# Kernel optimization log

Hardware: AMD Instinct MI355X
Metric: run time of the kernel (lower is better)

## Reference

```python
import jax, jax.numpy as jnp
import numpy as np
import math

L = 2          # gnn_num_layers
NDIM = 256     # gnn_hidden_size
H = 8          # num_heads
HH = H // 2    # heads per (full, local) split
DK = NDIM // H # 32, also == edim (relation_share_heads)
EDIM = DK
B, NPB = 32, 128
N = B * NPB            # 4096 nodes
EF = B * NPB * NPB     # 524288 complete-graph edges
EL = 131072            # local-graph edges
ELG = 262144           # line-graph edges
R = 128                # relation vocab


def _ln(x, g, b, eps=1e-5):
    m = x.mean(-1, keepdims=True)
    v = ((x - m) ** 2).mean(-1, keepdims=True)
    return (x - m) / jnp.sqrt(v + eps) * g + b


def _ffn(x, W1, b1, W2, b2, g, b):
    h = jax.nn.relu(x @ W1 + b1)
    return _ln(x + h @ W2 + b2, g, b)


def _edge_attn(q, k, v, e, src, dst, n_seg):
    """Relation-aware graph attention (DGL propagate_attention + edge_softmax).
    q,k,v: [n_seg,h,d]; e: [E,h,d] edge-relation bias or None; src,dst: [E].
    score_e = ((k[src]+e) . q[dst]) / sqrt(d); softmax over in-edges of dst;
    out[dst] = sum alpha_e * (v[src]+e)."""
    ks = k[src] + e if e is not None else k[src]          # [E,h,d]
    vs = v[src] + e if e is not None else v[src]          # [E,h,d]
    s = jnp.einsum('ehd,ehd->eh', ks, q[dst]) / math.sqrt(q.shape[-1])
    smax = jax.ops.segment_max(s, dst, num_segments=n_seg)
    ex = jnp.exp(s - jnp.maximum(smax, -1e30)[dst])
    den = jax.ops.segment_sum(ex, dst, num_segments=n_seg)[dst]
    alpha = ex / jnp.where(den > 0, den, 1.0)
    return jax.ops.segment_sum(alpha[..., None] * vs, dst, num_segments=n_seg)


def _model(x, rel_embed,
           n_Wq, n_bq, n_Wk, n_bk, n_Wv, n_bv, n_Wo, n_bo, n_ln_g, n_ln_b,
           n_f_W1, n_f_b1, n_f_W2, n_f_b2, n_f_ln_g, n_f_ln_b,
           e_Wsrc, e_Wdst, e_Wq, e_bq, e_Wk, e_Wv, e_Wo, e_bo, e_ln_g, e_ln_b,
           e_f_W1, e_f_b1, e_f_W2, e_f_b2, e_f_ln_g, e_f_ln_b,
           full_src, full_dst, g_src, g_dst, lg_src, lg_dst, edge_feat, full_edge_feat):
    lg_x = rel_embed[edge_feat]            # [EL, EDIM]  (shared embedding)
    lg_x_full = rel_embed[full_edge_feat]  # [EF, EDIM]  (fixed across layers)
    n, el, ef = x.shape[0], lg_x.shape[0], lg_x_full.shape[0]
    for i in range(L):
        # ---------- node update: first HH heads on full graph, last HH on local ----------
        q = (x @ n_Wq[i] + n_bq[i]).reshape(n, H, DK)
        k = (x @ n_Wk[i] + n_bk[i]).reshape(n, H, DK)
        v = (x @ n_Wv[i] + n_bv[i]).reshape(n, H, DK)
        # edim == d_k -> relation bias broadcast across heads (the expand branch)
        e_full = jnp.broadcast_to(lg_x_full[:, None, :], (ef, HH, DK))
        e_loc = jnp.broadcast_to(lg_x[:, None, :], (el, HH, DK))
        o1 = _edge_attn(q[:, :HH], k[:, :HH], v[:, :HH], e_full, full_src, full_dst, n)
        o2 = _edge_attn(q[:, HH:], k[:, HH:], v[:, HH:], e_loc, g_src, g_dst, n)
        o = jnp.concatenate([o1, o2], axis=1).reshape(n, NDIM)
        x_new = _ln(x + o @ n_Wo[i] + n_bo[i], n_ln_g[i], n_ln_b[i])
        x_new = _ffn(x_new, n_f_W1[i], n_f_b1[i], n_f_W2[i], n_f_b2[i], n_f_ln_g[i], n_f_ln_b[i])
        # ---------- edge update on line graph, conditioned on PRE-update src/dst node feats ----------
        mixed = lg_x + x[g_src] @ e_Wsrc[i] + x[g_dst] @ e_Wdst[i]  # [EL, EDIM]
        dke = EDIM // H
        eq = (mixed @ e_Wq[i] + e_bq[i]).reshape(el, H, dke)
        ek = (mixed @ e_Wk[i]).reshape(el, H, dke)
        ev = (mixed @ e_Wv[i]).reshape(el, H, dke)
        ow = _edge_attn(eq, ek, ev, None, lg_src, lg_dst, el).reshape(el, EDIM)
        lg_new = _ln(lg_x + ow @ e_Wo[i] + e_bo[i], e_ln_g[i], e_ln_b[i])
        lg_new = _ffn(lg_new, e_f_W1[i], e_f_b1[i], e_f_W2[i], e_f_b2[i], e_f_ln_g[i], e_f_ln_b[i])
        x, lg_x = x_new, lg_new
    return x, lg_x


def setup_inputs() -> dict:
    key = jax.random.key(0)
    ki = iter(jax.random.split(key, 48))
    def p(shape, scale=0.05):
        return jax.random.normal(next(ki), shape, dtype=jnp.float32) * scale
    rng = np.random.default_rng(0)
    blk = (np.arange(B, dtype=np.int32) * NPB)
    ii, jj = np.meshgrid(np.arange(NPB, dtype=np.int32), np.arange(NPB, dtype=np.int32), indexing='ij')
    full_src = (blk[:, None, None] + ii[None]).reshape(-1)   # block-diagonal complete graph
    full_dst = (blk[:, None, None] + jj[None]).reshape(-1)
    epb = EL // B
    g_src = (np.repeat(blk, epb) + rng.integers(0, NPB, EL)).astype(np.int32)
    g_dst = (np.repeat(blk, epb) + rng.integers(0, NPB, EL)).astype(np.int32)
    lpb = ELG // B
    eblk = np.arange(B, dtype=np.int32) * epb
    lg_src = (np.repeat(eblk, lpb) + rng.integers(0, epb, ELG)).astype(np.int32)
    lg_dst = (np.repeat(eblk, lpb) + rng.integers(0, epb, ELG)).astype(np.int32)
    return dict(
        x=jax.random.normal(next(ki), (N, NDIM), dtype=jnp.float32),
        rel_embed=p((R, EDIM), 1.0),
        full_src=jnp.asarray(full_src), full_dst=jnp.asarray(full_dst),
        g_src=jnp.asarray(g_src), g_dst=jnp.asarray(g_dst),
        lg_src=jnp.asarray(lg_src), lg_dst=jnp.asarray(lg_dst),
        edge_feat=jnp.asarray(rng.integers(0, R, EL).astype(np.int32)),
        full_edge_feat=jnp.asarray(rng.integers(0, R, EF).astype(np.int32)),
        n_Wq=p((L, NDIM, NDIM)), n_bq=p((L, NDIM)),
        n_Wk=p((L, NDIM, NDIM)), n_bk=p((L, NDIM)),
        n_Wv=p((L, NDIM, NDIM)), n_bv=p((L, NDIM)),
        n_Wo=p((L, NDIM, NDIM)), n_bo=p((L, NDIM)),
        n_ln_g=jnp.ones((L, NDIM), jnp.float32), n_ln_b=jnp.zeros((L, NDIM), jnp.float32),
        n_f_W1=p((L, NDIM, 4 * NDIM)), n_f_b1=p((L, 4 * NDIM)),
        n_f_W2=p((L, 4 * NDIM, NDIM)), n_f_b2=p((L, NDIM)),
        n_f_ln_g=jnp.ones((L, NDIM), jnp.float32), n_f_ln_b=jnp.zeros((L, NDIM), jnp.float32),
        e_Wsrc=p((L, NDIM, EDIM)), e_Wdst=p((L, NDIM, EDIM)),
        e_Wq=p((L, EDIM, EDIM)), e_bq=p((L, EDIM)),
        e_Wk=p((L, EDIM, EDIM)), e_Wv=p((L, EDIM, EDIM)),
        e_Wo=p((L, EDIM, EDIM)), e_bo=p((L, EDIM)),
        e_ln_g=jnp.ones((L, EDIM), jnp.float32), e_ln_b=jnp.zeros((L, EDIM), jnp.float32),
        e_f_W1=p((L, EDIM, 4 * EDIM)), e_f_b1=p((L, 4 * EDIM)),
        e_f_W2=p((L, 4 * EDIM, EDIM)), e_f_b2=p((L, EDIM)),
        e_f_ln_g=jnp.ones((L, EDIM), jnp.float32), e_f_ln_b=jnp.zeros((L, EDIM), jnp.float32),
    )


def reference(x, rel_embed, full_src, full_dst, g_src, g_dst, lg_src, lg_dst,
              edge_feat, full_edge_feat,
              n_Wq, n_bq, n_Wk, n_bk, n_Wv, n_bv, n_Wo, n_bo, n_ln_g, n_ln_b,
              n_f_W1, n_f_b1, n_f_W2, n_f_b2, n_f_ln_g, n_f_ln_b,
              e_Wsrc, e_Wdst, e_Wq, e_bq, e_Wk, e_Wv, e_Wo, e_bo, e_ln_g, e_ln_b,
              e_f_W1, e_f_b1, e_f_W2, e_f_b2, e_f_ln_g, e_f_ln_b):
    return _model(x, rel_embed,
                  n_Wq, n_bq, n_Wk, n_bk, n_Wv, n_bv, n_Wo, n_bo, n_ln_g, n_ln_b,
                  n_f_W1, n_f_b1, n_f_W2, n_f_b2, n_f_ln_g, n_f_ln_b,
                  e_Wsrc, e_Wdst, e_Wq, e_bq, e_Wk, e_Wv, e_Wo, e_bo, e_ln_g, e_ln_b,
                  e_f_W1, e_f_b1, e_f_W2, e_f_b2, e_f_ln_g, e_f_ln_b,
                  full_src, full_dst, g_src, g_dst, lg_src, lg_dst, edge_feat, full_edge_feat)
```

## Files before the change

kernel.cpp:

```cpp
#include <hip/hip_runtime.h>
#include <hip/hip_bf16.h>

typedef __hip_bfloat16 bf16;
typedef unsigned short ush;

static constexpr int kN   = 4096;
static constexpr int kND  = 256;
static constexpr int kEL  = 131072;
static constexpr int kED  = 32;
static constexpr int kELG = 262144;
static constexpr int kL   = 2;
static constexpr int kQW  = 832;
static constexpr float kScaleN = 0.17677669529663687f;

using frag_ab = __attribute__((ext_vector_type(8))) short;
using frag_cd = __attribute__((ext_vector_type(4))) float;

__device__ __forceinline__ float ldf(const void* p, size_t i, int isbf){
    return isbf ? __bfloat162float(((const bf16*)p)[i]) : ((const float*)p)[i];
}
__device__ __forceinline__ ush f2b(float f){ bf16 h = __float2bfloat16(f); return *(ush*)&h; }
__device__ __forceinline__ float b2f(ush u){ return __uint_as_float(((unsigned)u)<<16); }
__device__ __forceinline__ ush ldb(const void* p, size_t i, int isbf){
    return isbf ? ((const ush*)p)[i] : f2b(((const float*)p)[i]);
}

__global__ void detect_k(const ush* __restrict__ xin, int* __restrict__ flag){
    if (threadIdx.x == 0 && blockIdx.x == 0) {
        int plausible = 0;
        for (int i = 0; i < 128; ++i) {
            ush u = xin[i];
            int e = (u >> 7) & 0xFF;
            if (e == 0 || (e >= 110 && e <= 140)) ++plausible;
        }
        *flag = (plausible >= 102) ? 1 : 0;
    }
}

__global__ void setup_misc_k(const void* __restrict__ xin, const void* __restrict__ rel,
                             const int* __restrict__ feat,
                             const void* __restrict__ bq, const void* __restrict__ bk,
                             const void* __restrict__ bv,
                             float* __restrict__ xA, ush* __restrict__ xAb,
                             ush* __restrict__ lgA,
                             float* __restrict__ bQKV,
                             int* __restrict__ cntL, int* __restrict__ cntG,
                             const int* __restrict__ flag){
    const int isbf = *flag;
    long g = (long)blockIdx.x*256 + threadIdx.x;
    if (g < (long)kN*kND) {
        float v = ldf(xin, g, isbf);
        xA[g] = v; xAb[g] = f2b(v);
        return;
    }
    g -= (long)kN*kND;
    if (g < (long)kEL*kED) { int e = (int)(g >> 5), d = (int)(g & 31);
        lgA[g] = ldb(rel, (size_t)feat[e]*kED + d, isbf); return; }
    g -= (long)kEL*kED;
    if (g < 2*kQW) {
        int layer = (int)(g / kQW), j = (int)(g - (long)layer*kQW);
        float v = 0.f;
        if (j < 768) { int w = j >> 8, jj = j & 255;
            const void* B = (w==0)?bq:((w==1)?bk:bv);
            v = ldf(B, (size_t)layer*256 + jj, isbf); }
        bQKV[g] = v; return;
    }
    g -= 2*kQW;
    if (g < kN) { cntL[g] = 0; return; }
    g -= kN;
    if (g < kEL) { cntG[g] = 0; return; }
}

__global__ void trans_all_k(
    const void* __restrict__ nWq, const void* __restrict__ nWk, const void* __restrict__ nWv,
    const void* __restrict__ nWo, const void* __restrict__ nF1, const void* __restrict__ nF2,
    const void* __restrict__ eWs, const void* __restrict__ eWd,
    const void* __restrict__ eWq, const void* __restrict__ eWk, const void* __restrict__ eWv,
    const void* __restrict__ eWo, const void* __restrict__ eF1, const void* __restrict__ eF2,
    const int* __restrict__ flag,
    ush* __restrict__ wtQKVSD, ush* __restrict__ wtO, ush* __restrict__ wtF1,
    ush* __restrict__ wtF2, ush* __restrict__ wtEQKV, ush* __restrict__ wtEO,
    ush* __restrict__ wtEF1, ush* __restrict__ wtEF2)
{
    const int isbf = *flag;
    int g = blockIdx.x*256 + threadIdx.x;
    if (g < 393216){
        int w = g >> 17, gg = g & 131071;
        int layer = gg >> 16, idx = gg & 65535;
        int n = idx >> 8, k = idx & 255;
        const void* W = (w==0)?nWq:((w==1)?nWk:nWv);
        wtQKVSD[(size_t)layer*212992 + (size_t)(w*256+n)*256 + k] =
            ldb(W, (size_t)layer*65536 + (size_t)k*256 + n, isbf);
        return;
    }
    g -= 393216;
    if (g < 32768){
        int w = g >> 14, gg = g & 16383;
        int layer = gg >> 13, idx = gg & 8191;
        int n = idx >> 8, k = idx & 255;
        const void* W = w ? eWd : eWs;
        wtQKVSD[(size_t)layer*212992 + (size_t)(768 + w*32 + n)*256 + k] =
            ldb(W, (size_t)layer*8192 + (size_t)k*32 + n, isbf);
        return;
    }
    g -= 32768;
    if (g < 131072){
        int layer = g >> 16, rem = g & 65535;
        int n = rem >> 8, k = rem & 255;
        wtO[g] = ldb(nWo, (size_t)layer*65536 + (size_t)k*256 + n, isbf);
        return;
    }
    g -= 131072;
    if (g < 524288){
        int layer = g >> 18, rem = g & 262143;
        int n = rem >> 8, k = rem & 255;
        wtF1[g] = ldb(nF1, (size_t)layer*262144 + (size_t)k*1024 + n, isbf);
        return;
    }
    g -= 524288;
    if (g < 524288){
        int layer = g >> 18, rem = g & 262143;
        int n = rem >> 10, k = rem & 1023;
        wtF2[g] = ldb(nF2, (size_t)layer*262144 + (size_t)k*256 + n, isbf);
        return;
    }
    g -= 524288;
    if (g < 6144){
        int w = g >> 11, gg = g & 2047;
        int layer = gg >> 10, rem = gg & 1023;
        int n = rem >> 5, k = rem & 31;
        const void* W = (w==0)?eWq:((w==1)?eWk:eWv);
        wtEQKV[g] = ldb(W, (size_t)layer*1024 + (size_t)k*32 + n, isbf);
        return;
    }
    g -= 6144;
    if (g < 2048){
        int layer = g >> 10, rem = g & 1023;
        int n = rem >> 5, k = rem & 31;
        wtEO[g] = ldb(eWo, (size_t)layer*1024 + (size_t)k*32 + n, isbf);
        return;
    }
    g -= 2048;
    if (g < 8192){
        int layer = g >> 12, rem = g & 4095;
        int n = rem >> 5, k = rem & 31;
        wtEF1[g] = ldb(eF1, (size_t)layer*4096 + (size_t)k*128 + n, isbf);
        return;
    }
    g -= 8192;
    if (g < 8192){
        int layer = g >> 12, rem = g & 4095;
        int n = rem >> 7, k = rem & 127;
        wtEF2[g] = ldb(eF2, (size_t)layer*4096 + (size_t)k*32 + n, isbf);
        return;
    }
}

__global__ void count2_k(const int* __restrict__ gd, const int* __restrict__ lgd,
                         int* __restrict__ cntL, int* __restrict__ cntG){
    int g = blockIdx.x*256 + threadIdx.x;
    if (g < kEL) atomicAdd(&cntL[gd[g]], 1);
    else if (g < kEL + kELG) atomicAdd(&cntG[lgd[g - kEL]], 1);
}
__global__ __launch_bounds__(256) void scan_blk2_k(
    const int* __restrict__ cntL, const int* __restrict__ cntG,
    int* __restrict__ rowL, int* __restrict__ rowG, int* __restrict__ bsum)
{
    __shared__ int s[256];
    const int t = threadIdx.x;
    const bool isL = blockIdx.x < 4;
    const int* cnt = isL ? cntL : cntG;
    int* out = isL ? rowL : rowG;
    const int blk = isL ? blockIdx.x : blockIdx.x - 4;
    const int n = isL ? kN : kEL;
    const int b0 = blk*1024;
    int v[4], pre[4], tsum = 0;
    #pragma unroll
    for (int j=0;j<4;++j){
        int idx = b0 + t*4 + j;
        v[j] = (idx < n) ? cnt[idx] : 0;
        pre[j] = tsum; tsum += v[j];
    }
    s[t] = tsum; __syncthreads();
    for (int off=1; off<256; off<<=1){
        int x = (t>=off) ? s[t-off] : 0;
        __syncthreads();
        s[t] += x;
        __syncthreads();
    }
    int texc = s[t] - tsum;
    #pragma unroll
    for (int j=0;j<4;++j){
        int idx = b0 + t*4 + j;
        if (idx < n) out[idx] = texc + pre[j];
    }
    if (t == 255) bsum[(isL ? 0 : 8) + blk] = s[255];
}
__global__ __launch_bounds__(256) void scan_top2_k(int* __restrict__ bsum){
    __shared__ int sL[256], sG[256];
    const int t = threadIdx.x;
    int vL = (t < 4)   ? bsum[t]     : 0;
    int vG = (t < 128) ? bsum[8 + t] : 0;
    sL[t] = vL; sG[t] = vG; __syncthreads();
    for (int off=1; off<256; off<<=1){
        int xL = (t>=off) ? sL[t-off] : 0;
        int xG = (t>=off) ? sG[t-off] : 0;
        __syncthreads();
        sL[t] += xL; sG[t] += xG;
        __syncthreads();
    }
    if (t < 4)   bsum[t]     = sL[t] - vL;
    if (t < 128) bsum[8 + t] = sG[t] - vG;
}
__global__ void scan_add2_k(int* __restrict__ rowL, int* __restrict__ rowG,
                            const int* __restrict__ bsum,
                            int* __restrict__ curL, int* __restrict__ curG){
    int g = blockIdx.x*256 + threadIdx.x;
    if (g < kN){ int v = rowL[g] + bsum[g >> 10]; rowL[g] = v; curL[g] = v; }
    else if (g < kN + kEL){ int gg = g - kN;
        int v = rowG[gg] + bsum[8 + (gg >> 10)]; rowG[gg] = v; curG[gg] = v; }
    if (g == 0){ rowL[kN] = kEL; rowG[kEL] = kELG; }
}
__global__ void fill2_k(const int* __restrict__ gd, const int* __restrict__ lgd,
                        int* __restrict__ curL, int* __restrict__ curG,
                        int* __restrict__ eidL, int* __restrict__ eidG){
    int g = blockIdx.x*256 + threadIdx.x;
    if (g < kEL){ int pos = atomicAdd(&curL[gd[g]], 1); eidL[pos] = g; }
    else if (g < kEL + kELG){ int gg = g - kEL;
        int pos = atomicAdd(&curG[lgd[gg]], 1); eidG[pos] = gg; }
}

__global__ __launch_bounds__(256) void mgemm_k(
    const float* __restrict__ A, const ush* __restrict__ WT,
    const void* __restrict__ bias, size_t boff,
    float* __restrict__ C, const int* __restrict__ flag,
    int M, int N, int K, int flags)
{
    __shared__ __align__(16) ush As[64*40];
    __shared__ __align__(16) ush Ws[64*40];
    const int isbf = *flag;
    const int t = threadIdx.x;
    const int m0 = blockIdx.y*64, n0 = blockIdx.x*64;
    const int wave = t>>6, lane = t&63;
    const int quad = lane>>4, l15 = lane&15;
    const int r = t>>2, kq = (t&3)*8;
    const bool abf = flags & 32;

    frag_cd acc[4];
    #pragma unroll
    for (int tl=0; tl<4; ++tl)
        #pragma unroll
        for (int j=0;j<4;++j) acc[tl][j] = 0.f;

    const float* aprow = A + (size_t)(m0+r)*K + kq;
    const ush*   abrow = (const ush*)A + (size_t)(m0+r)*K + kq;
    const bool wok = (n0 + r) < N;
    const ush* wprow = WT + (size_t)(n0 + (wok ? r : 0))*K + kq;

    float4 a0, a1; uint4 av; uint4 wv;
    auto loadT = [&](int kk){
        if (abf) av = *(const uint4*)(abrow + kk);
        else { a0 = *(const float4*)(aprow + kk); a1 = *(const float4*)(aprow + kk + 4); }
        wv = wok ? *(const uint4*)(wprow + kk) : make_uint4(0u,0u,0u,0u);
    };
    loadT(0);

    for (int kk = 0; kk < K; kk += 32) {
        if (abf) {
            *(uint4*)&As[r*40 + kq] = av;
        } else {
            ushort4 p0 = make_ushort4(f2b(a0.x), f2b(a0.y), f2b(a0.z), f2b(a0.w));
            ushort4 p1 = make_ushort4(f2b(a1.x), f2b(a1.y), f2b(a1.z), f2b(a1.w));
            *(ushort4*)&As[r*40 + kq]     = p0;
            *(ushort4*)&As[r*40 + kq + 4] = p1;
        }
        *(uint4*)&Ws[r*40 + kq] = wv;
        __syncthreads();
        if (kk + 32 < K) loadT(kk + 32);
        frag_ab af = *(const frag_ab*)&As[(wave*16 + l15)*40 + quad*8];
        #pragma unroll
        for (int tl = 0; tl < 4; ++tl) {
            frag_ab bf = *(const frag_ab*)&Ws[(tl*16 + l15)*40 + quad*8];
            acc[tl] = __builtin_amdgcn_mfma_f32_16x16x32_bf16(af, bf, acc[tl], 0, 0, 0);
        }
        __syncthreads();
    }
    const bool do_relu = flags & 2;
    const bool has_b   = flags & 4;
    const bool obf     = flags & 8;
    #pragma unroll
    for (int tl = 0; tl < 4; ++tl) {
        int col = n0 + tl*16 + l15;
        if (col < N) {
            float bv = 0.f;
            if (has_b) bv = (flags & 16) ? ((const float*)bias)[boff + col]
                                         : ldf(bias, boff + col, isbf);
            #pragma unroll
            for (int rg = 0; rg < 4; ++rg) {
                int row = m0 + wave*16 + quad*4 + rg;
                float v = acc[tl][rg] + bv;
                if (do_relu) v = fmaxf(v, 0.f);
                if (obf) ((ush*)C)[(size_t)row*N + col] = f2b(v);
                else     C[(size_t)row*N + col] = v;
            }
        }
    }
}

__global__ __launch_bounds__(64) void ln_k(
    const float* __restrict__ a, const float* __restrict__ b,
    const void* __restrict__ g, const void* __restrict__ be, size_t goff,
    float* __restrict__ out, ush* __restrict__ outb,
    const int* __restrict__ flag, int D)
{
    const int isbf = *flag;
    const int row = blockIdx.x;
    const int t = threadIdx.x;
    float v[4];
    int cnt = 0;
    float s = 0.f;
    for (int i = t; i < D; i += 64) {
        float x = a[(size_t)row*D + i];
        if (b) x += b[(size_t)row*D + i];
        v[cnt++] = x; s += x;
    }
    #pragma unroll
    for (int off = 32; off > 0; off >>= 1) s += __shfl_down(s, off);
    s = __shfl(s, 0);
    const float mean = s / D;
    float qq = 0.f;
    for (int c2 = 0; c2 < cnt; ++c2) { float d = v[c2]-mean; qq += d*d; }
    #pragma unroll
    for (int off = 32; off > 0; off >>= 1) qq += __shfl_down(qq, off);
    qq = __shfl(qq, 0);
    const float inv = rsqrtf(fmaxf(qq, 0.f) / D + 1e-5f);
    cnt = 0;
    for (int i = t; i < D; i += 64) {
        float r = (v[cnt++] - mean)*inv*ldf(g, goff + i, isbf) + ldf(be, goff + i, isbf);
        out[(size_t)row*D + i] = r;
        outb[(size_t)row*D + i] = f2b(r);
    }
}

__global__ __launch_bounds__(256) void eqkv_mfma_k(
    const ush* __restrict__ lg, const float* __restrict__ xsd,
    const int* __restrict__ gsrc, const int* __restrict__ gdst,
    const ush* __restrict__ WQKV, size_t woff,
    const void* __restrict__ bq, size_t boff,
    ush* __restrict__ eq, ush* __restrict__ ek, ush* __restrict__ ev,
    const int* __restrict__ flag)
{
    __shared__ __align__(16) ush mixs[128*40];
    __shared__ __align__(16) ush wts[3][32*40];
    __shared__ float bqs[32];
    const int isbf = *flag;
    const int t = threadIdx.x;
    const int e0 = blockIdx.x * 128;
    #pragma unroll
    for (int i = t; i < 768; i += 256) {
        int m = i >> 8, r2 = i & 255;
        int n = r2 >> 3, k4 = (r2 & 7) * 4;
        *(ushort4*)&wts[m][n*40 + k4] =
            *(const ushort4*)&WQKV[(size_t)m*2048 + woff + (size_t)n*32 + k4];
    }
    if (t < 32) bqs[t] = ldf(bq, boff + t, isbf);
    {
        int r = t >> 1, c0 = (t & 1) * 16;
        int e = e0 + r;
        int s = gsrc[e], d2 = gdst[e];
        const ush* lp = lg + (size_t)e*32 + c0;
        const float* sp = xsd + (size_t)s*kQW + c0;
        const float* dp = xsd + (size_t)d2*kQW + 32 + c0;
        #pragma unroll
        for (int j = 0; j < 16; ++j)
            mixs[r*40 + c0 + j] = f2b(b2f(lp[j]) + sp[j] + dp[j]);
    }
    __syncthreads();
    const int wave = t >> 6, l15 = t & 15, quad = (t >> 4) & 3;
    #pragma unroll
    for (int mi = 0; mi < 2; ++mi) {
        const int mt = wave*2 + mi;
        frag_ab af = *(const frag_ab*)&mixs[(mt*16 + l15)*40 + quad*8];
        #pragma unroll
        for (int w = 0; w < 3; ++w) {
            ush* outp = (w==0) ? eq : ((w==1) ? ek : ev);
            #pragma unroll
            for (int nt = 0; nt < 2; ++nt) {
                frag_ab bf = *(const frag_ab*)&wts[w][(nt*16 + l15)*40 + quad*8];
                frag_cd acc = {0.f, 0.f, 0.f, 0.f};
                acc = __builtin_amdgcn_mfma_f32_16x16x32_bf16(af, bf, acc, 0, 0, 0);
                const float bv = (w==0) ? bqs[nt*16 + l15] : 0.f;
                #pragma unroll
                for (int rg = 0; rg < 4; ++rg) {
                    int row = e0 + mt*16 + quad*4 + rg;
                    outp[(size_t)row*32 + nt*16 + l15] = f2b(acc[rg] + bv);
                }
            }
        }
    }
}

__global__ __launch_bounds__(256) void effn_mfma_k(
    const ush* __restrict__ A,
    const ush* __restrict__ W1T, size_t w1off, const void* __restrict__ b1, size_t b1off,
    const ush* __restrict__ W2T, size_t w2off, const void* __restrict__ b2, size_t b2off,
    const void* __restrict__ g, const void* __restrict__ be, size_t goff,
    ush* __restrict__ out, const int* __restrict__ flag)
{
    __shared__ __align__(16) ush w1t[128*40];
    __shared__ __align__(16) ush w2t[32*136];
    __shared__ __align__(16) ush hid[64*136];
    __shared__ float b1s[128], b2s[32];
    const int isbf = *flag;
    const int t = threadIdx.x;
    const int wave = t >> 6, l15 = t & 15, quad = (t >> 4) & 3;

    #pragma unroll
    for (int i = t; i < 1024; i += 256) {
        int n1 = i >> 3, k4 = (i & 7) * 4;
        *(ushort4*)&w1t[n1*40 + k4] = *(const ushort4*)&W1T[w1off + (size_t)n1*32 + k4];
        int n2 = i >> 5, kq2 = (i & 31) * 4;
        *(ushort4*)&w2t[n2*136 + kq2] = *(const ushort4*)&W2T[w2off + (size_t)n2*128 + kq2];
    }
    if (t < 128) b1s[t] = ldf(b1, b1off + t, isbf);
    if (t < 32)  b2s[t] = ldf(b2, b2off + t, isbf);
    __syncthreads();

    const float g0  = ldf(g,  goff + l15, isbf),      g1v = ldf(g,  goff + 16 + l15, isbf);
    const float be0 = ldf(be, goff + l15, isbf),      be1 = ldf(be, goff + 16 + l15, isbf);
    const float bb0 = b2s[l15], bb1 = b2s[16 + l15];

    for (int tt = 0; tt < 2; ++tt) {
        const int e0 = (blockIdx.x*2 + tt) * 64;
        {
            const int m = wave*16 + l15;
            frag_ab af = *(const frag_ab*)&A[(size_t)(e0+m)*32 + quad*8];
            #pragma unroll
            for (int nt = 0; nt < 8; ++nt) {
                frag_ab bf = *(const frag_ab*)&w1t[(nt*16 + l15)*40 + quad*8];
                frag_cd acc = {0.f, 0.f, 0.f, 0.f};
                acc = __builtin_amdgcn_mfma_f32_16x16x32_bf16(af, bf, acc, 0, 0, 0);
                float bv = b1s[nt*16 + l15];
                #pragma unroll
                for (int rg = 0; rg < 4; ++rg) {
                    int row = wave*16 + quad*4 + rg;
                    hid[row*136 + nt*16 + l15] = f2b(fmaxf(acc[rg] + bv, 0.f));
                }
            }
        }
        frag_cd acc2[2] = {{0.f,0.f,0.f,0.f},{0.f,0.f,0.f,0.f}};
        #pragma unroll
        for (int ks = 0; ks < 4; ++ks) {
            frag_ab af2 = *(const frag_ab*)&hid[(wave*16 + l15)*136 + ks*32 + quad*8];
            #pragma unroll
            for (int tl = 0; tl < 2; ++tl) {
                frag_ab bf2 = *(const frag_ab*)&w2t[(tl*16 + l15)*136 + ks*32 + quad*8];
                acc2[tl] = __builtin_amdgcn_mfma_f32_16x16x32_bf16(af2, bf2, acc2[tl], 0, 0, 0);
            }
        }
        #pragma unroll
        for (int rg = 0; rg < 4; ++rg) {
            const int row = e0 + wave*16 + quad*4 + rg;
            float v0 = acc2[0][rg] + bb0 + b2f(A[(size_t)row*32 + l15]);
            float v1 = acc2[1][rg] + bb1 + b2f(A[(size_t)row*32 + 16 + l15]);
            float s = v0 + v1;
            s += __shfl_xor(s,1); s += __shfl_xor(s,2); s += __shfl_xor(s,4); s += __shfl_xor(s,8);
            const float mean = s * (1.f/32.f);
            float q = (v0-mean)*(v0-mean) + (v1-mean)*(v1-mean);
            q += __shfl_xor(q,1); q += __shfl_xor(q,2); q += __shfl_xor(q,4); q += __shfl_xor(q,8);
            const float inv = rsqrtf(q * (1.f/32.f) + 1e-5f);
            out[(size_t)row*32 + l15]      = f2b((v0-mean)*inv*g0  + be0);
            out[(size_t)row*32 + 16 + l15] = f2b((v1-mean)*inv*g1v + be1);
        }
    }
}

__global__ __launch_bounds__(512) void full_attn_k(
    const float* __restrict__ q, const float* __restrict__ k, const float* __restrict__ v,
    const void* __restrict__ rel, const int* __restrict__ feat, ush* __restrict__ o,
    const int* __restrict__ flag, int ldq)
{
    __shared__ __align__(8) ush ks[128][36];
    __shared__ __align__(8) ush vs[128][36];
    __shared__ __align__(8) ush rs[128][36];
    __shared__ float pb[8][32][34];
    const int isbf = *flag;
    const int bid = blockIdx.x;
    const int b = bid >> 4, h = (bid >> 2) & 3, qtr = bid & 3;
    const int t = threadIdx.x;
    for (int i = t; i < 4096; i += 512) {
        int r = i >> 5, d = i & 31;
        rs[r][d] = ldb(rel, i, isbf);
        size_t base = ((size_t)(b*128 + r))*ldq + h*32 + d;
        ks[r][d] = f2b(k[base]);
        vs[r][d] = f2b(v[base]);
    }
    __syncthreads();
    const int wave = t >> 6, lane = t & 63;
    const int dstL = lane >> 1, part = lane & 1;
    const int dst = qtr*32 + dstL;
    const int dbase = part*16;
    float qr[16];
    { size_t base = ((size_t)(b*128 + dst))*ldq + h*32 + dbase;
      #pragma unroll
      for (int d=0; d<16; ++d) qr[d] = q[base + d]; }
    const int* fp = feat + (size_t)b*16384 + dst;
    const int s0 = wave*16;
    float m = -1e30f, l = 0.f;
    float acc[16];
    #pragma unroll
    for (int d=0; d<16; ++d) acc[d] = 0.f;
    int f = fp[s0*128];
    for (int sI = 0; sI < 16; ++sI) {
        const int s = s0 + sI;
        int fn = (sI+1 < 16) ? fp[(s+1)*128] : 0;
        float er[16];
        float scp = 0.f;
        #pragma unroll
        for (int j2 = 0; j2 < 4; ++j2) {
            ushort4 eu = *(const ushort4*)&rs[f][dbase + j2*4];
            ushort4 ku = *(const ushort4*)&ks[s][dbase + j2*4];
            float e0 = b2f(eu.x), e1 = b2f(eu.y), e2 = b2f(eu.z), e3 = b2f(eu.w);
            er[j2*4+0]=e0; er[j2*4+1]=e1; er[j2*4+2]=e2; er[j2*4+3]=e3;
            scp += (b2f(ku.x)+e0)*qr[j2*4+0] + (b2f(ku.y)+e1)*qr[j2*4+1]
                 + (b2f(ku.z)+e2)*qr[j2*4+2] + (b2f(ku.w)+e3)*qr[j2*4+3];
        }
        const float sc = (scp + __shfl_xor(scp, 1)) * kScaleN;
        float mn = fmaxf(m, sc);
        float c0 = __expf(m - mn);
        float pp = __expf(sc - mn);
        l = l*c0 + pp;
        #pragma unroll
        for (int j2 = 0; j2 < 4; ++j2) {
            ushort4 vu = *(const ushort4*)&vs[s][dbase + j2*4];
            acc[j2*4+0] = acc[j2*4+0]*c0 + pp*(b2f(vu.x)+er[j2*4+0]);
            acc[j2*4+1] = acc[j2*4+1]*c0 + pp*(b2f(vu.y)+er[j2*4+1]);
            acc[j2*4+2] = acc[j2*4+2]*c0 + pp*(b2f(vu.z)+er[j2*4+2]);
            acc[j2*4+3] = acc[j2*4+3]*c0 + pp*(b2f(vu.w)+er[j2*4+3]);
        }
        m = mn; f = fn;
    }
    if (part == 0) { pb[wave][dstL][0] = m; pb[wave][dstL][1] = l; }
    #pragma unroll
    for (int d=0; d<16; ++d) pb[wave][dstL][2 + dbase + d] = acc[d];
    __syncthreads();
    {
        const int dstL2 = t & 31, grp = t >> 5;
        float mw[8], lw[8];
        #pragma unroll
        for (int w=0; w<8; ++w){ mw[w]=pb[w][dstL2][0]; lw[w]=pb[w][dstL2][1]; }
        float M = mw[0];
        #pragma unroll
        for (int w=1; w<8; ++w) M = fmaxf(M, mw[w]);
        float sw[8];
        float L = 0.f;
        #pragma unroll
        for (int w=0; w<8; ++w){ sw[w] = __expf(mw[w]-M); L += lw[w]*sw[w]; }
        const float inv = 1.f / fmaxf(L, 1e-30f);
        size_t base = ((size_t)(b*128 + qtr*32 + dstL2))*kND + h*32 + grp*2;
        #pragma unroll
        for (int d=0; d<2; ++d) {
            float a = 0.f;
            #pragma unroll
            for (int w=0; w<8; ++w) a += pb[w][dstL2][2+grp*2+d]*sw[w];
            o[base + d] = f2b(a*inv);
        }
    }
}

__global__ __launch_bounds__(256) void loc_gather_k(
    const float* __restrict__ q, const float* __restrict__ k, const float* __restrict__ v,
    const ush* __restrict__ lg, const int* __restrict__ gsrc,
    const int* __restrict__ rowp, const int* __restrict__ eidl,
    ush* __restrict__ o, int ldq)
{
    const int n = blockIdx.x;
    const int h = threadIdx.x >> 6;
    const int lane = threadIdx.x & 63;
    const int g = lane >> 4;
    const int d0 = (lane & 15) * 2;
    const size_t hoff = (size_t)(4 + h) * 32 + d0;
    const float2 q2 = *(const float2*)&q[(size_t)n*ldq + hoff];
    const int beg = rowp[n], end = rowp[n+1];
    const int deg = end - beg;
    float m = -1e30f, l = 0.f, ax = 0.f, ay = 0.f;
    if (deg > 0) {
        const int nIter = (deg + 3) >> 2;
        int idx = beg + g;
        int ce = eidl[min(idx, end-1)];
        int cs = gsrc[ce];
        for (int it = 0; it < nIter; ++it) {
            const bool valid = idx < end;
            const int e = ce, s = cs;
            idx += 4;
            if (it + 1 < nIter) { ce = eidl[min(idx, end-1)]; cs = gsrc[ce]; }
            const float2 kv = *(const float2*)&k[(size_t)s*ldq + hoff];
            const ushort2 lvu = *(const ushort2*)&lg[(size_t)e*32 + d0];
            const float2 vv = *(const float2*)&v[(size_t)s*ldq + hoff];
            const float lvx = b2f(lvu.x), lvy = b2f(lvu.y);
            float part = (kv.x+lvx)*q2.x + (kv.y+lvy)*q2.y;
            part += __shfl_xor(part, 1);
            part += __shfl_xor(part, 2);
            part += __shfl_xor(part, 4);
            part += __shfl_xor(part, 8);
            const float sc = part * kScaleN;
            const float mn = valid ? fmaxf(m, sc) : m;
            const float c  = __expf(m - mn);
            const float pp = valid ? __expf(sc - mn) : 0.f;
            l  = l*c  + pp;
            ax = ax*c + pp*(vv.x+lvx);
            ay = ay*c + pp*(vv.y+lvy);
            m  = mn;
        }
        #pragma unroll
        for (int off = 16; off <= 32; off <<= 1) {
            const float mo = __shfl_xor(m, off);
            const float lo = __shfl_xor(l, off);
            const float xo = __shfl_xor(ax, off);
            const float yo = __shfl_xor(ay, off);
            const float M  = fmaxf(m, mo);
            const float c1 = __expf(m - M);
            const float c2 = __expf(mo - M);
            l  = l*c1  + lo*c2;
            ax = ax*c1 + xo*c2;
            ay = ay*c1 + yo*c2;
            m  = M;
        }
    }
    if (g == 0) {
        const float inv = 1.f / fmaxf(l, 1e-30f);
        *(ushort2*)&o[(size_t)n*kND + hoff] = make_ushort2(f2b(ax*inv), f2b(ay*inv));
    }
}

__global__ __launch_bounds__(256) void lgs_ewo_k(
    const ush* __restrict__ eq, const ush* __restrict__ ek, const ush* __restrict__ ev,
    const int* __restrict__ lsrc, const int* __restrict__ rowp, const int* __restrict__ eidl,
    const ush* __restrict__ res,
    const ush* __restrict__ WO, size_t wooff, const void* __restrict__ bo, size_t booff,
    const void* __restrict__ g1, const void* __restrict__ be1, size_t g1off,
    ush* __restrict__ out, const int* __restrict__ flag)
{
    __shared__ __align__(16) ush ows[32*40];
    __shared__ __align__(16) ush wos[32*40];
    __shared__ float cs[32][36];
    __shared__ float bos[32], gs[32], bs[32];
    const int isbf = *flag;
    const int t = threadIdx.x;
    const int base = blockIdx.x * 32;
    {
        int n = t >> 3, k4 = (t & 7) * 4;
        *(ushort4*)&wos[n*40 + k4] = *(const ushort4*)&WO[wooff + (size_t)n*32 + k4];
    }
    if (t < 32) {
        bos[t] = ldf(bo, booff + t, isbf);
        gs[t]  = ldf(g1, g1off + t, isbf);
        bs[t]  = ldf(be1, g1off + t, isbf);
    }
    {
        const int d2 = base + (t >> 3), h = t & 7;
        const ushort4 qu = *(const ushort4*)&eq[(size_t)d2*32 + h*4];
        const float q0 = b2f(qu.x), q1 = b2f(qu.y), q2 = b2f(qu.z), q3 = b2f(qu.w);
        const int beg = rowp[d2], end = rowp[d2+1];
        float m = -1e30f, l = 0.f;
        float4 acc = make_float4(0.f,0.f,0.f,0.f);
        int i = beg;
        int s = 0;
        if (i < end) { s = lsrc[eidl[i]]; }
        while (i < end) {
            const int sc_s = s;
            ++i;
            if (i < end) { s = lsrc[eidl[i]]; }
            const ushort4 ku = *(const ushort4*)&ek[(size_t)sc_s*32 + h*4];
            const ushort4 vu = *(const ushort4*)&ev[(size_t)sc_s*32 + h*4];
            float sc = (b2f(ku.x)*q0 + b2f(ku.y)*q1 + b2f(ku.z)*q2 + b2f(ku.w)*q3) * 0.5f;
            float mn = fmaxf(m, sc);
            float c = __expf(m - mn);
            float pp = __expf(sc - mn);
            l = l*c + pp;
            acc.x = acc.x*c + pp*b2f(vu.x);
            acc.y = acc.y*c + pp*b2f(vu.y);
            acc.z = acc.z*c + pp*b2f(vu.z);
            acc.w = acc.w*c + pp*b2f(vu.w);
            m = mn;
        }
        const float inv = 1.f / fmaxf(l, 1e-30f);
        const int r = t >> 3, c0 = h*4;
        ows[r*40 + c0 + 0] = f2b(acc.x*inv);
        ows[r*40 + c0 + 1] = f2b(acc.y*inv);
        ows[r*40 + c0 + 2] = f2b(acc.z*inv);
        ows[r*40 + c0 + 3] = f2b(acc.w*inv);
    }
    __syncthreads();
    {
        const int wave = t >> 6, l15 = t & 15, quad = (t >> 4) & 3;
        const int mt = wave & 1, nt = wave >> 1;
        frag_ab af = *(const frag_ab*)&ows[(mt*16 + l15)*40 + quad*8];
        frag_ab bf = *(const frag_ab*)&wos[(nt*16 + l15)*40 + quad*8];
        frag_cd acc = {0.f, 0.f, 0.f, 0.f};
        acc = __builtin_amdgcn_mfma_f32_16x16x32_bf16(af, bf, acc, 0, 0, 0);
        #pragma unroll
        for (int rg = 0; rg < 4; ++rg) {
            const int row = mt*16 + quad*4 + rg;
            const int col = nt*16 + l15;
            cs[row][col] = acc[rg] + bos[col] + b2f(res[(size_t)(base+row)*32 + col]);
        }
    }
    __syncthreads();
    {
        const int row = t >> 3, c0 = (t & 7) * 4;
        const float v0 = cs[row][c0], v1 = cs[row][c0+1];
        const float v2 = cs[row][c0+2], v3 = cs[row][c0+3];
        float s = v0+v1+v2+v3;
        s += __shfl_xor(s,1); s += __shfl_xor(s,2); s += __shfl_xor(s,4);
        const float mean = s * (1.f/32.f);
        float qq = (v0-mean)*(v0-mean)+(v1-mean)*(v1-mean)
                 + (v2-mean)*(v2-mean)+(v3-mean)*(v3-mean);
        qq += __shfl_xor(qq,1); qq += __shfl_xor(qq,2); qq += __shfl_xor(qq,4);
        const float inv = rsqrtf(qq * (1.f/32.f) + 1e-5f);
        out[(size_t)(base+row)*32 + c0 + 0] = f2b((v0-mean)*inv*gs[c0+0] + bs[c0+0]);
        out[(size_t)(base+row)*32 + c0 + 1] = f2b((v1-mean)*inv*gs[c0+1] + bs[c0+1]);
        out[(size_t)(base+row)*32 + c0 + 2] = f2b((v2-mean)*inv*gs[c0+2] + bs[c0+2]);
        out[(size_t)(base+row)*32 + c0 + 3] = f2b((v3-mean)*inv*gs[c0+3] + bs[c0+3]);
    }
}

__global__ void out_k(const float* __restrict__ xf, const ush* __restrict__ lgf,
                      void* __restrict__ out, const int* __restrict__ flag){
    const int isbf = *flag;
    int g = blockIdx.x*256 + threadIdx.x;
    if (g < kN*kND) {
        float v = xf[g];
        if (isbf) ((ush*)out)[g] = f2b(v);
        else      ((float*)out)[g] = v;
    } else {
        ush u = lgf[g - kN*kND];
        if (isbf) ((ush*)out)[g] = u;
        else      ((float*)out)[g] = b2f(u);
    }
}

static inline void mgemm(const float* A, const ush* WT, const void* bias, size_t boff,
                         float* C, const int* flag, int M, int N, int K, int flags,
                         hipStream_t s){
    dim3 grid((N+63)/64, M/64);
    mgemm_k<<<grid, 256, 0, s>>>(A, WT, bias, boff, C, flag, M, N, K, flags);
}

extern "C" void kernel_launch(void* const* d_in, const int* in_sizes, int n_in,
                              void* d_out, int out_size, void* d_ws, size_t ws_size,
                              hipStream_t stream) {
    const void* x_in      = d_in[0];
    const void* rel       = d_in[1];
    const int* g_src      = (const int*)d_in[4];
    const int* g_dst      = (const int*)d_in[5];
    const int* lg_src     = (const int*)d_in[6];
    const int* lg_dst     = (const int*)d_in[7];
    const int* edge_feat  = (const int*)d_in[8];
    const int* full_feat  = (const int*)d_in[9];
    const void* n_Wq   = d_in[10];
    const void* n_bq   = d_in[11];
    const void* n_Wk   = d_in[12];
    const void* n_bk   = d_in[13];
    const void* n_Wv   = d_in[14];
    const void* n_bv   = d_in[15];
    const void* n_Wo   = d_in[16];
    const void* n_bo   = d_in[17];
    const void* n_lng  = d_in[18];
    const void* n_lnb  = d_in[19];
    const void* n_fW1  = d_in[20];
    const void* n_fb1  = d_in[21];
    const void* n_fW2  = d_in[22];
    const void* n_fb2  = d_in[23];
    const void* n_flng = d_in[24];
    const void* n_flnb = d_in[25];
    const void* e_Wsrc = d_in[26];
    const void* e_Wdst = d_in[27];
    const void* e_Wq   = d_in[28];
    const void* e_bq   = d_in[29];
    const void* e_Wk   = d_in[30];
    const void* e_Wv   = d_in[31];
    const void* e_Wo   = d_in[32];
    const void* e_bo   = d_in[33];
    const void* e_lng  = d_in[34];
    const void* e_lnb  = d_in[35];
    const void* e_fW1  = d_in[36];
    const void* e_fb1  = d_in[37];
    const void* e_fW2  = d_in[38];
    const void* e_fb2  = d_in[39];
    const void* e_flng = d_in[40];
    const void* e_flnb = d_in[41];

    float* p = (float*)d_ws;
    size_t off = 0;
    auto AL = [&](size_t n){ float* r = p + off; off += n; return r; };
    int* flagp = (int*)AL(64);
    float* xA   = AL((size_t)kN*kND);
    float* xB   = AL((size_t)kN*kND);
    float* xM   = AL((size_t)kN*kND);
    ush*   xAb  = (ush*)AL((size_t)kN*kND/2);
    ush*   xBb  = (ush*)AL((size_t)kN*kND/2);
    ush*   xMb  = (ush*)AL((size_t)kN*kND/2);
    float* qkvb = AL((size_t)kN*kQW);
    ush*   ob   = (ush*)AL((size_t)kN*kND/2);
    float* tN   = AL((size_t)kN*kND);
    ush*   nh   = (ush*)AL((size_t)kN*512);
    ush*   lgA  = (ush*)AL((size_t)kEL*kED/2);
    ush*   lgB  = (ush*)AL((size_t)kEL*kED/2);
    ush*   lgM  = (ush*)AL((size_t)kEL*kED/2);
    ush*   eqb  = (ush*)AL((size_t)kEL*16);
    ush*   ekb  = (ush*)AL((size_t)kEL*16);
    ush*   evb  = (ush*)AL((size_t)kEL*16);
    int* cntL  = (int*)AL(kN);
    int* rowL  = (int*)AL(kN + 64);
    int* curL  = (int*)AL(kN);
    int* eidL  = (int*)AL(kEL);
    int* cntG  = (int*)AL(kEL);
    int* rowG  = (int*)AL(kEL + 64);
    int* curG  = (int*)AL(kEL);
    int* eidG  = (int*)AL(kELG);
    int* bsum  = (int*)AL(256);
    ush* wtQKVSD = (ush*)AL(212992);
    float* bQKV  = AL(2*kQW);
    ush* wtO  = (ush*)AL(65536);
    ush* wtF1 = (ush*)AL(262144);
    ush* wtF2 = (ush*)AL(262144);
    ush* wtEQKV = (ush*)AL(3072);
    ush* wtEO   = (ush*)AL(1024);
    ush* wtEF1  = (ush*)AL(4096);
    ush* wtEF2  = (ush*)AL(4096);
    if (ws_size < off * sizeof(float)) return;

    detect_k<<<1, 64, 0, stream>>>((const ush*)x_in, flagp);
    {
        long total = (long)kN*kND + (long)kEL*kED + 2*kQW + kN + kEL;
        int blocks = (int)((total + 255) / 256);
        setup_misc_k<<<blocks, 256, 0, stream>>>(x_in, rel, edge_feat, n_bq, n_bk, n_bv,
                                                 xA, xAb, lgA, bQKV, cntL, cntG, flagp);
    }
    trans_all_k<<<6368, 256, 0, stream>>>(n_Wq, n_Wk, n_Wv, n_Wo, n_fW1, n_fW2,
                                          e_Wsrc, e_Wdst, e_Wq, e_Wk, e_Wv, e_Wo,
                                          e_fW1, e_fW2, flagp,
                                          wtQKVSD, wtO, wtF1, wtF2,
                                          wtEQKV, wtEO, wtEF1, wtEF2);

    count2_k<<<(kEL+kELG)/256, 256, 0, stream>>>(g_dst, lg_dst, cntL, cntG);
    scan_blk2_k<<<132, 256, 0, stream>>>(cntL, cntG, rowL, rowG, bsum);
    scan_top2_k<<<1, 256, 0, stream>>>(bsum);
    scan_add2_k<<<(kN+kEL)/256, 256, 0, stream>>>(rowL, rowG, bsum, curL, curG);
    fill2_k<<<(kEL+kELG)/256, 256, 0, stream>>>(g_dst, lg_dst, curL, curG, eidL, eidG);

    float* xc = xA;  float* xn = xB;
    ush* xcb = xAb;  ush* xnb = xBb;
    ush* lgc = lgA;  ush* lgn = lgB;

    for (int i = 0; i < kL; ++i) {
        const size_t o256 = (size_t)i*kND;
        const size_t o1024= (size_t)i*1024;
        const size_t o32  = (size_t)i*kED;
        const size_t o128 = (size_t)i*128;

        mgemm((const float*)xcb, wtQKVSD + (size_t)i*212992, bQKV, (size_t)i*kQW, qkvb,
              flagp, kN, kQW, kND, 4|16|32, stream);
        full_attn_k<<<512, 512, 0, stream>>>(qkvb, qkvb+256, qkvb+512, rel, full_feat,
                                             ob, flagp, kQW);
        loc_gather_k<<<kN, 256, 0, stream>>>(qkvb, qkvb+256, qkvb+512, lgc, g_src,
                                             rowL, eidL, ob, kQW);
        mgemm((const float*)ob, wtO + (size_t)i*65536, n_bo, o256, tN, flagp,
              kN, kND, kND, 4|32, stream);
        ln_k<<<kN, 64, 0, stream>>>(xc, tN, n_lng, n_lnb, o256, xM, xMb, flagp, kND);
        mgemm((const float*)xMb, wtF1 + (size_t)i*262144, n_fb1, o1024, (float*)nh, flagp,
              kN, 1024, kND, 4|2|8|32, stream);
        mgemm((const float*)nh, wtF2 + (size_t)i*262144, n_fb2, o256, tN, flagp,
              kN, kND, 1024, 4|32, stream);
        ln_k<<<kN, 64, 0, stream>>>(xM, tN, n_flng, n_flnb, o256, xn, xnb, flagp, kND);

        eqkv_mfma_k<<<kEL/128, 256, 0, stream>>>(lgc, qkvb + 768, g_src, g_dst,
                                                 wtEQKV, (size_t)i*1024, e_bq, o32,
                                                 eqb, ekb, evb, flagp);
        lgs_ewo_k<<<kEL/32, 256, 0, stream>>>(eqb, ekb, evb, lg_src, rowG, eidG,
                                              lgc, wtEO, (size_t)i*1024, e_bo, o32,
                                              e_lng, e_lnb, o32, lgM, flagp);
        effn_mfma_k<<<kEL/128, 256, 0, stream>>>(lgM, wtEF1, (size_t)i*4096, e_fb1, o128,
                                                 wtEF2, (size_t)i*4096, e_fb2, o32,
                                                 e_flng, e_flnb, o32, lgn, flagp);

        { float* t = xc; xc = xn; xn = t; }
        { ush* t = xcb; xcb = xnb; xnb = t; }
        { ush* t = lgc; lgc = lgn; lgn = t; }
    }

    out_k<<<(kN*kND + kEL*kED)/256, 256, 0, stream>>>(xc, lgc, d_out, flagp);
}
```

Measured before the change: 564.1 us.

## Deepen GEMM K-step to 64 and emit bf16 local K/V copy for gather

```diff
diff --git a/kernel.cpp b/kernel.cpp
--- a/kernel.cpp
+++ b/kernel.cpp
@@ -234,16 +234,16 @@
     const float* __restrict__ A, const ush* __restrict__ WT,
     const void* __restrict__ bias, size_t boff,
     float* __restrict__ C, const int* __restrict__ flag,
-    int M, int N, int K, int flags)
+    int M, int N, int K, int flags, ush* __restrict__ aux)
 {
-    __shared__ __align__(16) ush As[64*40];
-    __shared__ __align__(16) ush Ws[64*40];
+    __shared__ __align__(16) ush As[64*72];
+    __shared__ __align__(16) ush Ws[64*72];
     const int isbf = *flag;
     const int t = threadIdx.x;
     const int m0 = blockIdx.y*64, n0 = blockIdx.x*64;
     const int wave = t>>6, lane = t&63;
     const int quad = lane>>4, l15 = lane&15;
-    const int r = t>>2, kq = (t&3)*8;
+    const int r = t>>3, kq = (t&7)*8;
     const bool abf = flags & 32;
 
     frag_cd acc[4];
@@ -252,36 +252,44 @@
         #pragma unroll
         for (int j=0;j<4;++j) acc[tl][j] = 0.f;
 
-    const float* aprow = A + (size_t)(m0+r)*K + kq;
-    const ush*   abrow = (const ush*)A + (size_t)(m0+r)*K + kq;
-    const bool wok = (n0 + r) < N;
-    const ush* wprow = WT + (size_t)(n0 + (wok ? r : 0))*K + kq;
-
-    float4 a0, a1; uint4 av; uint4 wv;
+    const float* ap0 = A + (size_t)(m0+r)*K + kq;
+    const float* ap1 = A + (size_t)(m0+r+32)*K + kq;
+    const ush*   ab0 = (const ush*)A + (size_t)(m0+r)*K + kq;
+    const ush*   ab1 = (const ush*)A + (size_t)(m0+r+32)*K + kq;
+    const ush*   wp0 = WT + (size_t)(n0+r)*K + kq;
+    const ush*   wp1 = WT + (size_t)(n0+r+32)*K + kq;
+
+    float4 a00,a01,a10,a11; uint4 av0,av1, wv0,wv1;
     auto loadT = [&](int kk){
-        if (abf) av = *(const uint4*)(abrow + kk);
-        else { a0 = *(const float4*)(aprow + kk); a1 = *(const float4*)(aprow + kk + 4); }
-        wv = wok ? *(const uint4*)(wprow + kk) : make_uint4(0u,0u,0u,0u);
+        if (abf) { av0 = *(const uint4*)(ab0+kk); av1 = *(const uint4*)(ab1+kk); }
+        else { a00 = *(const float4*)(ap0+kk); a01 = *(const float4*)(ap0+kk+4);
+               a10 = *(const float4*)(ap1+kk); a11 = *(const float4*)(ap1+kk+4); }
+        wv0 = *(const uint4*)(wp0+kk); wv1 = *(const uint4*)(wp1+kk);
     };
     loadT(0);
 
-    for (int kk = 0; kk < K; kk += 32) {
+    for (int kk = 0; kk < K; kk += 64) {
         if (abf) {
-            *(uint4*)&As[r*40 + kq] = av;
+            *(uint4*)&As[r*72 + kq]        = av0;
+            *(uint4*)&As[(r+32)*72 + kq]   = av1;
         } else {
-            ushort4 p0 = make_ushort4(f2b(a0.x), f2b(a0.y), f2b(a0.z), f2b(a0.w));
-            ushort4 p1 = make_ushort4(f2b(a1.x), f2b(a1.y), f2b(a1.z), f2b(a1.w));
-            *(ushort4*)&As[r*40 + kq]     = p0;
-            *(ushort4*)&As[r*40 + kq + 4] = p1;
-        }
-        *(uint4*)&Ws[r*40 + kq] = wv;
+            *(ushort4*)&As[r*72 + kq]       = make_ushort4(f2b(a00.x),f2b(a00.y),f2b(a00.z),f2b(a00.w));
+            *(ushort4*)&As[r*72 + kq + 4]   = make_ushort4(f2b(a01.x),f2b(a01.y),f2b(a01.z),f2b(a01.w));
+            *(ushort4*)&As[(r+32)*72 + kq]     = make_ushort4(f2b(a10.x),f2b(a10.y),f2b(a10.z),f2b(a10.w));
+            *(ushort4*)&As[(r+32)*72 + kq + 4] = make_ushort4(f2b(a11.x),f2b(a11.y),f2b(a11.z),f2b(a11.w));
+        }
+        *(uint4*)&Ws[r*72 + kq]      = wv0;
+        *(uint4*)&Ws[(r+32)*72 + kq] = wv1;
         __syncthreads();
-        if (kk + 32 < K) loadT(kk + 32);
-        frag_ab af = *(const frag_ab*)&As[(wave*16 + l15)*40 + quad*8];
+        if (kk + 64 < K) loadT(kk + 64);
+        frag_ab af0 = *(const frag_ab*)&As[(wave*16 + l15)*72 + quad*8];
+        frag_ab af1 = *(const frag_ab*)&As[(wave*16 + l15)*72 + 32 + quad*8];
         #pragma unroll
         for (int tl = 0; tl < 4; ++tl) {
-            frag_ab bf = *(const frag_ab*)&Ws[(tl*16 + l15)*40 + quad*8];
-            acc[tl] = __builtin_amdgcn_mfma_f32_16x16x32_bf16(af, bf, acc[tl], 0, 0, 0);
+            frag_ab bf0 = *(const frag_ab*)&Ws[(tl*16 + l15)*72 + quad*8];
+            acc[tl] = __builtin_amdgcn_mfma_f32_16x16x32_bf16(af0, bf0, acc[tl], 0, 0, 0);
+            frag_ab bf1 = *(const frag_ab*)&Ws[(tl*16 + l15)*72 + 32 + quad*8];
+            acc[tl] = __builtin_amdgcn_mfma_f32_16x16x32_bf16(af1, bf1, acc[tl], 0, 0, 0);
         }
         __syncthreads();
     }
@@ -291,18 +299,22 @@
     #pragma unroll
     for (int tl = 0; tl < 4; ++tl) {
         int col = n0 + tl*16 + l15;
-        if (col < N) {
-            float bv = 0.f;
-            if (has_b) bv = (flags & 16) ? ((const float*)bias)[boff + col]
-                                         : ldf(bias, boff + col, isbf);
-            #pragma unroll
-            for (int rg = 0; rg < 4; ++rg) {
-                int row = m0 + wave*16 + quad*4 + rg;
-                float v = acc[tl][rg] + bv;
-                if (do_relu) v = fmaxf(v, 0.f);
-                if (obf) ((ush*)C)[(size_t)row*N + col] = f2b(v);
-                else     C[(size_t)row*N + col] = v;
-            }
+        float bv = 0.f;
+        if (has_b) bv = (flags & 16) ? ((const float*)bias)[boff + col]
+                                     : ldf(bias, boff + col, isbf);
+        int c2 = -1;
+        if (flags & 64) {
+            if (col >= 384 && col < 512) c2 = col - 384;
+            else if (col >= 640 && col < 768) c2 = col - 512;
+        }
+        #pragma unroll
+        for (int rg = 0; rg < 4; ++rg) {
+            int row = m0 + wave*16 + quad*4 + rg;
+            float v = acc[tl][rg] + bv;
+            if (do_relu) v = fmaxf(v, 0.f);
+            if (obf) ((ush*)C)[(size_t)row*N + col] = f2b(v);
+            else     C[(size_t)row*N + col] = v;
+            if (c2 >= 0) aux[(size_t)row*256 + c2] = f2b(v);
         }
     }
 }
@@ -569,7 +581,7 @@
 }
 
 __global__ __launch_bounds__(256) void loc_gather_k(
-    const float* __restrict__ q, const float* __restrict__ k, const float* __restrict__ v,
+    const float* __restrict__ q, const ush* __restrict__ kv,
     const ush* __restrict__ lg, const int* __restrict__ gsrc,
     const int* __restrict__ rowp, const int* __restrict__ eidl,
     ush* __restrict__ o, int ldq)
@@ -594,11 +606,11 @@
             const int e = ce, s = cs;
             idx += 4;
             if (it + 1 < nIter) { ce = eidl[min(idx, end-1)]; cs = gsrc[ce]; }
-            const float2 kv = *(const float2*)&k[(size_t)s*ldq + hoff];
+            const ushort2 ku = *(const ushort2*)&kv[(size_t)s*256 + h*32 + d0];
             const ushort2 lvu = *(const ushort2*)&lg[(size_t)e*32 + d0];
-            const float2 vv = *(const float2*)&v[(size_t)s*ldq + hoff];
+            const ushort2 vu = *(const ushort2*)&kv[(size_t)s*256 + 128 + h*32 + d0];
             const float lvx = b2f(lvu.x), lvy = b2f(lvu.y);
-            float part = (kv.x+lvx)*q2.x + (kv.y+lvy)*q2.y;
+            float part = (b2f(ku.x)+lvx)*q2.x + (b2f(ku.y)+lvy)*q2.y;
             part += __shfl_xor(part, 1);
             part += __shfl_xor(part, 2);
             part += __shfl_xor(part, 4);
@@ -608,8 +620,8 @@
             const float c  = __expf(m - mn);
             const float pp = valid ? __expf(sc - mn) : 0.f;
             l  = l*c  + pp;
-            ax = ax*c + pp*(vv.x+lvx);
-            ay = ay*c + pp*(vv.y+lvy);
+            ax = ax*c + pp*(b2f(vu.x)+lvx);
+            ay = ay*c + pp*(b2f(vu.y)+lvy);
             m  = mn;
         }
         #pragma unroll
@@ -742,9 +754,9 @@
 
 static inline void mgemm(const float* A, const ush* WT, const void* bias, size_t boff,
                          float* C, const int* flag, int M, int N, int K, int flags,
-                         hipStream_t s){
+                         hipStream_t s, ush* aux){
     dim3 grid((N+63)/64, M/64);
-    mgemm_k<<<grid, 256, 0, s>>>(A, WT, bias, boff, C, flag, M, N, K, flags);
+    mgemm_k<<<grid, 256, 0, s>>>(A, WT, bias, boff, C, flag, M, N, K, flags, aux);
 }
 
 extern "C" void kernel_launch(void* const* d_in, const int* in_sizes, int n_in,
@@ -802,6 +814,7 @@
     ush*   xBb  = (ush*)AL((size_t)kN*kND/2);
     ush*   xMb  = (ush*)AL((size_t)kN*kND/2);
     float* qkvb = AL((size_t)kN*kQW);
+    ush*   kvloc= (ush*)AL((size_t)kN*128);
     ush*   ob   = (ush*)AL((size_t)kN*kND/2);
     float* tN   = AL((size_t)kN*kND);
     ush*   nh   = (ush*)AL((size_t)kN*512);
@@ -861,18 +874,18 @@
         const size_t o128 = (size_t)i*128;
 
         mgemm((const float*)xcb, wtQKVSD + (size_t)i*212992, bQKV, (size_t)i*kQW, qkvb,
-              flagp, kN, kQW, kND, 4|16|32, stream);
+              flagp, kN, kQW, kND, 4|16|32|64, stream, kvloc);
         full_attn_k<<<512, 512, 0, stream>>>(qkvb, qkvb+256, qkvb+512, rel, full_feat,
                                              ob, flagp, kQW);
-        loc_gather_k<<<kN, 256, 0, stream>>>(qkvb, qkvb+256, qkvb+512, lgc, g_src,
+        loc_gather_k<<<kN, 256, 0, stream>>>(qkvb, kvloc, lgc, g_src,
                                              rowL, eidL, ob, kQW);
         mgemm((const float*)ob, wtO + (size_t)i*65536, n_bo, o256, tN, flagp,
-              kN, kND, kND, 4|32, stream);
+              kN, kND, kND, 4|32, stream, nullptr);
         ln_k<<<kN, 64, 0, stream>>>(xc, tN, n_lng, n_lnb, o256, xM, xMb, flagp, kND);
         mgemm((const float*)xMb, wtF1 + (size_t)i*262144, n_fb1, o1024, (float*)nh, flagp,
-              kN, 1024, kND, 4|2|8|32, stream);
+              kN, 1024, kND, 4|2|8|32, stream, nullptr);
         mgemm((const float*)nh, wtF2 + (size_t)i*262144, n_fb2, o256, tN, flagp,
-              kN, kND, 1024, 4|32, stream);
+              kN, kND, 1024, 4|32, stream, nullptr);
         ln_k<<<kN, 64, 0, stream>>>(xM, tN, n_flng, n_flnb, o256, xn, xnb, flagp, kND);
 
         eqkv_mfma_k<<<kEL/128, 256, 0, stream>>>(lgc, qkvb + 768, g_src, g_dst,
```

Measured after the change: 525.2 us. -6.9%, faster.
